# Kernel tuning notes

Hardware: AMD Instinct MI355X
Metric: run time of the kernel (lower is better)

Reference implementation:

```python
import jax, jax.numpy as jnp
import numpy as np

B, CIN, T, H, W = 2, 512, 8, 32, 32
COUT = 512

def conv2d(x, w, b):
    # x: (B, C, H, W), w: (O, I, kh, kw) -> (B, O, H, W), SAME padding
    y = jax.lax.conv_general_dilated(x, w, (1, 1), 'SAME',
        dimension_numbers=('NCHW', 'OIHW', 'NCHW'))
    return y + b[None, :, None, None]

def convlstm(x, w, b, wci, wcf, wco):
    # x: (B, C, T, H, W) -> (B, Cout, T, H, W); peepholes wci/wcf/wco: (Cout, H, W)
    bb, c, t, hh, ww = x.shape
    cout = wci.shape[0]
    h0 = jnp.zeros((bb, cout, hh, ww), x.dtype)

    def step(carry, xt):
        Hp, Cp = carry
        z = conv2d(jnp.concatenate([xt, Hp], axis=1), w, b)  # (B, 4*Cout, H, W)
        ic, fc, cc, oc = jnp.split(z, 4, axis=1)
        i = jax.nn.sigmoid(ic + wci * Cp)
        f = jax.nn.sigmoid(fc + wcf * Cp)
        Cn = f * Cp + i * jax.nn.relu(cc)   # activation='relu'
        o = jax.nn.sigmoid(oc + wco * Cn)
        Hn = o * jax.nn.relu(Cn)
        return (Hn, Cn), Hn

    (_, _), hs = jax.lax.scan(step, (h0, h0), jnp.moveaxis(x, 2, 0))
    return jnp.moveaxis(hs, 0, 2)  # (B, Cout, T, H, W)

def setup_inputs():
    key = jax.random.key(0)
    ks = jax.random.split(key, 16)
    inp = {'x': jax.random.normal(ks[0], (B, CIN, T, H, W), jnp.float32)}
    for l in range(3):
        k = ks[1 + 5 * l: 6 + 5 * l]
        inp['conv_w%d' % (l + 1)] = jax.random.normal(k[0], (4 * COUT, CIN + COUT, 3, 3), jnp.float32) * 0.02
        inp['conv_b%d' % (l + 1)] = jnp.zeros((4 * COUT,), jnp.float32)
        inp['wci%d' % (l + 1)] = jax.random.normal(k[1], (COUT, H, W), jnp.float32) * 0.02
        inp['wcf%d' % (l + 1)] = jax.random.normal(k[2], (COUT, H, W), jnp.float32) * 0.02
        inp['wco%d' % (l + 1)] = jax.random.normal(k[3], (COUT, H, W), jnp.float32) * 0.02
    return inp

def reference(x, conv_w1, conv_b1, wci1, wcf1, wco1,
              conv_w2, conv_b2, wci2, wcf2, wco2,
              conv_w3, conv_b3, wci3, wcf3, wco3):
    y = convlstm(x, conv_w1, conv_b1, wci1, wcf1, wco1)
    y = convlstm(y, conv_w2, conv_b2, wci2, wcf2, wco2)
    y = convlstm(y, conv_w3, conv_b3, wci3, wcf3, wco3)
    # Sigmoid on last time step: output[:, :, -1] -> (B, Cout, H, W)
    return jax.nn.sigmoid(y[:, :, -1])
```

## Files before the change

### kernel.cpp

```cpp
#include <hip/hip_runtime.h>

typedef unsigned short u16;
typedef __bf16 bf16x8 __attribute__((ext_vector_type(8)));
typedef float f32x4 __attribute__((ext_vector_type(4)));

#define T_STEPS 8
#define PLANE 1156
#define ROWB 2176

__device__ __forceinline__ u16 f2bf(float f) {
    unsigned u = __float_as_uint(f);
    return (u16)((u + 0x7fff + ((u >> 16) & 1)) >> 16);
}
__device__ __forceinline__ float sigmoidf(float x) {
    return 1.f / (1.f + expf(-x));
}
__device__ __forceinline__ void gl_lds16(const void* g, void* l) {
    __builtin_amdgcn_global_load_lds(
        (const __attribute__((address_space(1))) void*)g,
        (__attribute__((address_space(3))) void*)l, 16, 0, 0);
}

__global__ void repack_w(const float* __restrict__ w,
                         u16* __restrict__ wx, u16* __restrict__ wh) {
    int g = blockIdx.x * 256 + threadIdx.x;
    int co_in = g & 127; g >>= 7;
    int quad  = g & 3;   g >>= 2;
    int kt    = g % 144; g /= 144;
    int co_blk = g & 15; g >>= 4;
    int part = g;
    int co = co_blk * 128 + co_in;
    int cc = kt / 9, r = kt - cc * 9;
    int ci = cc * 32 + quad * 8;
    const float* src = w + ((size_t)co * 1024 + (size_t)part * 512 + ci) * 9 + r;
    u16* dst = (part ? wh : wx) +
               ((((size_t)co_blk * 144 + kt) * 4 + quad) * 128 + co_in) * 8;
    union { u16 u[8]; uint4 v; } tmp;
#pragma unroll
    for (int j = 0; j < 8; j++) tmp.u[j] = f2bf(src[(size_t)j * 9]);
    *(uint4*)dst = tmp.v;
}

__global__ __launch_bounds__(256) void pretransform_x(
    const float* __restrict__ x, u16* __restrict__ Xp) {
    const int bt = blockIdx.x >> 5;
    const int y  = blockIdx.x & 31;
    const int b  = bt >> 3;
    const int xx = threadIdx.x & 31, cg0 = threadIdx.x >> 5;
    const float* src = x + ((size_t)(b * 512) * T_STEPS + (bt & 7)) * 1024
                         + y * 32 + xx;
    u16* dst = Xp + (((size_t)bt * 34 + y + 1) * 34 + (xx + 1)) * 512;
#pragma unroll
    for (int it = 0; it < 8; ++it) {
        const int cig = cg0 + it * 8;
        union { u16 u[8]; uint4 v; } pk;
#pragma unroll
        for (int j = 0; j < 8; ++j)
            pk.u[j] = f2bf(src[(size_t)(cig * 8 + j) * 8192]);
        *(uint4*)(dst + cig * 8) = pk.v;
    }
}

template<bool XMODE>
__global__ __launch_bounds__(512, 4) void conv_gemm(
    const u16* __restrict__ Wp, const u16* __restrict__ Xp, int t0,
    float* __restrict__ Z, int ldz) {
    __shared__ __align__(16) u16 Bt[2][6528];

    const int tid = threadIdx.x;
    const int GX  = XMODE ? 32 : 16;
    const int nwg = GX * 16;
    const int bid = blockIdx.y * GX + blockIdx.x;
    const int swz = (bid & 7) * (nwg >> 3) + (bid >> 3);
    const int co_blk = swz / GX;
    const int nblk   = swz - co_blk * GX;
    const int n0 = nblk * 128;

    const int wave = tid >> 6, lane = tid & 63;
    const int wm = wave >> 1, wn = wave & 1;
    const int q_l = lane >> 4, m_l = lane & 15;

    const int plane = n0 >> 10;
    const int bb_ = XMODE ? (plane & 1) : plane;
    const int tt  = XMODE ? (t0 + (plane >> 1)) : t0;
    const int pyb = (n0 & 1023) >> 5;
    const u16* pbase = Xp + (size_t)(bb_ * T_STEPS + tt) * PLANE * 512;

    const int c0 = tid;
    const int p0 = c0 >> 2, sl0 = c0 & 3;
    const int yl0 = p0 / 34, xl0 = p0 - yl0 * 34;
    const int src0 = ((pyb + yl0) * 34 + xl0) * 512 + ((sl0 ^ ((xl0 >> 1) & 3)) << 3);
    const int c1 = 512 + tid;
    const int p1 = c1 >> 2, sl1 = c1 & 3;
    const int yl1 = p1 / 34, xl1 = p1 - yl1 * 34;
    const int src1 = ((pyb + yl1) * 34 + xl1) * 512 + ((sl1 ^ ((xl1 >> 1) & 3)) << 3);
    const bool do1 = tid < 304;

    const bf16x8* Aq = (const bf16x8*)(const void*)
        ((const uint4*)(Wp + (size_t)co_blk * 144 * 4096)
         + (q_l * 128 + wm * 32 + m_l));

    int colb[2][3];
#pragma unroll
    for (int xh = 0; xh < 2; xh++)
#pragma unroll
        for (int rx = 0; rx < 3; rx++) {
            int xl = xh * 16 + m_l + rx;
            colb[xh][rx] = xl * 64 + ((q_l ^ ((xl >> 1) & 3)) << 4);
        }
    const int wnrow = wn * 2 * ROWB;

    f32x4 acc[2][4];
#pragma unroll
    for (int i = 0; i < 2; i++)
#pragma unroll
        for (int j = 0; j < 4; j++) acc[i][j] = (f32x4){0.f, 0.f, 0.f, 0.f};

    gl_lds16(pbase + src0, &Bt[0][c0 * 8]);
    if (do1) gl_lds16(pbase + src1, &Bt[0][c1 * 8]);
    bf16x8 areg[3][2];
    areg[0][0] = Aq[0];          areg[0][1] = Aq[16];
    areg[1][0] = Aq[512];        areg[1][1] = Aq[512 + 16];

    for (int cc = 0; cc < 16; ++cc) {
        const int cb = cc & 1;
        const char* btc = (const char*)&Bt[cb][0];
#pragma unroll
        for (int r = 0; r < 9; ++r) {
            const int kt = cc * 9 + r;
            if (r == 0) {
                asm volatile("" ::: "memory");
                asm volatile("s_waitcnt vmcnt(4)" ::: "memory");
                __builtin_amdgcn_s_barrier();
                asm volatile("" ::: "memory");
            }
            if (cc < 15 || r < 7) {
                areg[(r + 2) % 3][0] = Aq[(size_t)(kt + 2) * 512];
                areg[(r + 2) % 3][1] = Aq[(size_t)(kt + 2) * 512 + 16];
            }
            if (r == 1 && cc < 15) {
                const u16* gs = pbase + (cc + 1) * 32;
                gl_lds16(gs + src0, &Bt[cb ^ 1][c0 * 8]);
                if (do1) gl_lds16(gs + src1, &Bt[cb ^ 1][c1 * 8]);
            }
            const int ry = r / 3, rx = r % 3;
            bf16x8 af0 = areg[r % 3][0];
            bf16x8 af1 = areg[r % 3][1];
            bf16x8 bf0 = *(const bf16x8*)(btc + wnrow + (0 + ry) * ROWB + colb[0][rx]);
            bf16x8 bf1 = *(const bf16x8*)(btc + wnrow + (0 + ry) * ROWB + colb[1][rx]);
            bf16x8 bf2 = *(const bf16x8*)(btc + wnrow + (1 + ry) * ROWB + colb[0][rx]);
            bf16x8 bf3 = *(const bf16x8*)(btc + wnrow + (1 + ry) * ROWB + colb[1][rx]);
            __builtin_amdgcn_s_setprio(1);
            acc[0][0] = __builtin_amdgcn_mfma_f32_16x16x32_bf16(af0, bf0, acc[0][0], 0, 0, 0);
            acc[0][1] = __builtin_amdgcn_mfma_f32_16x16x32_bf16(af0, bf1, acc[0][1], 0, 0, 0);
            acc[0][2] = __builtin_amdgcn_mfma_f32_16x16x32_bf16(af0, bf2, acc[0][2], 0, 0, 0);
            acc[0][3] = __builtin_amdgcn_mfma_f32_16x16x32_bf16(af0, bf3, acc[0][3], 0, 0, 0);
            acc[1][0] = __builtin_amdgcn_mfma_f32_16x16x32_bf16(af1, bf0, acc[1][0], 0, 0, 0);
            acc[1][1] = __builtin_amdgcn_mfma_f32_16x16x32_bf16(af1, bf1, acc[1][1], 0, 0, 0);
            acc[1][2] = __builtin_amdgcn_mfma_f32_16x16x32_bf16(af1, bf2, acc[1][2], 0, 0, 0);
            acc[1][3] = __builtin_amdgcn_mfma_f32_16x16x32_bf16(af1, bf3, acc[1][3], 0, 0, 0);
            __builtin_amdgcn_s_setprio(0);
        }
    }

#pragma unroll
    for (int mt = 0; mt < 2; mt++)
#pragma unroll
        for (int nt = 0; nt < 4; nt++)
#pragma unroll
            for (int reg = 0; reg < 4; reg++) {
                int co = co_blk * 128 + wm * 32 + mt * 16 + q_l * 4 + reg;
                int n  = n0 + wn * 64 + nt * 16 + m_l;
                float* zp = &Z[(size_t)co * ldz + n];
                if (XMODE) *zp = acc[mt][nt][reg];
                else       *zp += acc[mt][nt][reg];
            }
}

__global__ __launch_bounds__(256) void gates_kernel(
    const float* __restrict__ zx, int nxoff,
    const float* __restrict__ bias,
    const float* __restrict__ wci, const float* __restrict__ wcf,
    const float* __restrict__ wco,
    float* __restrict__ C, int is_first,
    u16* __restrict__ Yp, int t,
    float* __restrict__ outp) {
    __shared__ u16 Hs[16][136];
    const int tid = threadIdx.x;
    const int s0  = blockIdx.x * 128;
    const int co0 = blockIdx.y * 16;
    const int b   = blockIdx.z;
    const int sl = tid & 127, ch = tid >> 7;
    const int s = s0 + sl;

#pragma unroll
    for (int k = 0; k < 8; ++k) {
        const int co = co0 + k * 2 + ch;
        const size_t zi_ = (size_t)co * 4096 + nxoff + b * 1024 + s;
        float zi = zx[zi_]                       + bias[co];
        float zf = zx[zi_ + (size_t)512 * 4096]  + bias[co + 512];
        float zc = zx[zi_ + (size_t)1024 * 4096] + bias[co + 1024];
        float zo = zx[zi_ + (size_t)1536 * 4096] + bias[co + 1536];
        const size_t ci_ = ((size_t)b * 512 + co) * 1024 + s;
        float Cp = is_first ? 0.f : C[ci_];
        const int ps = co * 1024 + s;
        float gi = sigmoidf(zi + wci[ps] * Cp);
        float gf = sigmoidf(zf + wcf[ps] * Cp);
        float Cn = gf * Cp + gi * fmaxf(zc, 0.f);
        float go = sigmoidf(zo + wco[ps] * Cn);
        float Hn = go * fmaxf(Cn, 0.f);
        C[ci_] = Cn;
        Hs[k * 2 + ch][sl] = f2bf(Hn);
        if (outp) outp[ci_] = sigmoidf(Hn);
    }
    __syncthreads();
    const int sl2 = tid & 127, half = tid >> 7;
    const int s2 = s0 + sl2;
    const int yp = (s2 >> 5) + 1, xp = (s2 & 31) + 1;
    u16* dst = Yp + (((size_t)(b * T_STEPS + t) * 34 + yp) * 34 + xp) * 512
                  + co0 + half * 8;
    union { u16 u[8]; uint4 v; } pk;
#pragma unroll
    for (int j = 0; j < 8; ++j) pk.u[j] = Hs[half * 8 + j][sl2];
    *(uint4*)dst = pk.v;
}

extern "C" void kernel_launch(void* const* d_in, const int* in_sizes, int n_in,
                              void* d_out, int out_size, void* d_ws, size_t ws_size,
                              hipStream_t stream) {
    const float* x = (const float*)d_in[0];

    char* ws = (char*)d_ws;
    size_t off = 0;
    auto carve = [&](size_t bytes) { char* p = ws + off; off += (bytes + 255) & ~(size_t)255; return p; };

    u16*   Wx   = (u16*)  carve((size_t)16 * 144 * 4096 * 2);
    u16*   Wh   = (u16*)  carve((size_t)16 * 144 * 4096 * 2);
    float* Zx   = (float*)carve((size_t)2048 * 4096 * 4);
    float* Cbuf = (float*)carve((size_t)2 * 512 * 1024 * 4);
    const size_t PADB = (size_t)16 * PLANE * 512 * 2;
    u16*   Yp1  = (u16*)  carve(PADB);
    u16*   Yp2  = (u16*)  carve(PADB);
    (void)ws_size; (void)in_sizes; (void)n_in; (void)out_size;

    hipMemsetAsync(Yp1, 0, PADB, stream);
    hipMemsetAsync(Yp2, 0, PADB, stream);
    pretransform_x<<<512, 256, 0, stream>>>(x, Yp2);

    for (int l = 0; l < 3; ++l) {
        const float* w    = (const float*)d_in[1 + 5 * l];
        const float* bias = (const float*)d_in[2 + 5 * l];
        const float* wci  = (const float*)d_in[3 + 5 * l];
        const float* wcf  = (const float*)d_in[4 + 5 * l];
        const float* wco  = (const float*)d_in[5 + 5 * l];
        const u16* inl = (l == 0) ? Yp2 : (l == 1 ? Yp1 : Yp2);
        u16* Ycur      = (l == 0) ? Yp1 : (l == 1 ? Yp2 : Yp1);

        repack_w<<<9216, 256, 0, stream>>>(w, Wx, Wh);

        for (int t = 0; t < T_STEPS; ++t) {
            if ((t & 1) == 0)
                conv_gemm<true><<<dim3(32, 16), 512, 0, stream>>>(
                    Wx, inl, t, Zx, 4096);
            if (t > 0)
                conv_gemm<false><<<dim3(16, 16), 512, 0, stream>>>(
                    Wh, Ycur, t - 1, Zx + (size_t)(t & 1) * 2048, 4096);
            float* outp = (l == 2 && t == T_STEPS - 1) ? (float*)d_out : nullptr;
            gates_kernel<<<dim3(8, 32, 2), 256, 0, stream>>>(
                Zx, (t & 1) * 2048, bias, wci, wcf, wco,
                Cbuf, (t == 0) ? 1 : 0, Ycur, t, outp);
        }
    }
}
```

Measured before the change: 2.266 ms.

## Double output-channel tile for input conv and double-buffer LDS B-fragment reads

The input-projection GEMM now computes 256 output channels per workgroup (MF=4) instead of 128, halving the grid and the number of times each activation tile is staged into LDS. The weight repack lays out the input half with a 256-channel block stride to match. B fragments from LDS are now prefetched one tap ahead into a register double buffer, and the barrier/waitcnt is hoisted per channel chunk with counts adjusted for the extra A loads. Launch bounds drop to 2 waves-per-EU occupancy to allow the larger accumulator and register footprint, trading occupancy for reuse.

New measurement: 2.214 ms. 2.3% less time.

```diff
diff --git a/kernel.cpp b/kernel.cpp
--- a/kernel.cpp
+++ b/kernel.cpp
@@ -24,17 +24,26 @@
 __global__ void repack_w(const float* __restrict__ w,
                          u16* __restrict__ wx, u16* __restrict__ wh) {
     int g = blockIdx.x * 256 + threadIdx.x;
-    int co_in = g & 127; g >>= 7;
-    int quad  = g & 3;   g >>= 2;
-    int kt    = g % 144; g /= 144;
-    int co_blk = g & 15; g >>= 4;
-    int part = g;
-    int co = co_blk * 128 + co_in;
+    const int HALF = 1179648;
+    int part = g >= HALF;
+    int gg = part ? g - HALF : g;
+    int co_in, co_blk, quad, kt, co; u16* dst;
+    if (!part) {
+        co_in = gg & 255; gg >>= 8;
+        quad  = gg & 3;   gg >>= 2;
+        kt = gg % 144; co_blk = gg / 144;
+        co = co_blk * 256 + co_in;
+        dst = wx + ((((size_t)co_blk * 144 + kt) * 4 + quad) * 256 + co_in) * 8;
+    } else {
+        co_in = gg & 127; gg >>= 7;
+        quad  = gg & 3;   gg >>= 2;
+        kt = gg % 144; co_blk = gg / 144;
+        co = co_blk * 128 + co_in;
+        dst = wh + ((((size_t)co_blk * 144 + kt) * 4 + quad) * 128 + co_in) * 8;
+    }
     int cc = kt / 9, r = kt - cc * 9;
     int ci = cc * 32 + quad * 8;
     const float* src = w + ((size_t)co * 1024 + (size_t)part * 512 + ci) * 9 + r;
-    u16* dst = (part ? wh : wx) +
-               ((((size_t)co_blk * 144 + kt) * 4 + quad) * 128 + co_in) * 8;
     union { u16 u[8]; uint4 v; } tmp;
 #pragma unroll
     for (int j = 0; j < 8; j++) tmp.u[j] = f2bf(src[(size_t)j * 9]);
@@ -61,19 +70,28 @@
     }
 }
 
+#define READB(dstv, btcp, rr) {                                              \
+    const int ry_ = (rr) / 3, rx_ = (rr) % 3;                                \
+    dstv[0] = *(const bf16x8*)((btcp) + wnrow + (0 + ry_) * ROWB + colb[0][rx_]); \
+    dstv[1] = *(const bf16x8*)((btcp) + wnrow + (0 + ry_) * ROWB + colb[1][rx_]); \
+    dstv[2] = *(const bf16x8*)((btcp) + wnrow + (1 + ry_) * ROWB + colb[0][rx_]); \
+    dstv[3] = *(const bf16x8*)((btcp) + wnrow + (1 + ry_) * ROWB + colb[1][rx_]); }
+
 template<bool XMODE>
-__global__ __launch_bounds__(512, 4) void conv_gemm(
+__global__ __launch_bounds__(512, 2) void conv_gemm(
     const u16* __restrict__ Wp, const u16* __restrict__ Xp, int t0,
     float* __restrict__ Z, int ldz) {
+    constexpr int MF   = XMODE ? 4 : 2;
+    constexpr int COIN = XMODE ? 256 : 128;
+    constexpr int KSTR = 4 * COIN;
+
     __shared__ __align__(16) u16 Bt[2][6528];
 
     const int tid = threadIdx.x;
-    const int GX  = XMODE ? 32 : 16;
-    const int nwg = GX * 16;
-    const int bid = blockIdx.y * GX + blockIdx.x;
-    const int swz = (bid & 7) * (nwg >> 3) + (bid >> 3);
-    const int co_blk = swz / GX;
-    const int nblk   = swz - co_blk * GX;
+    const int bid = blockIdx.y * (XMODE ? 32 : 16) + blockIdx.x;
+    const int swz = (bid & 7) * 32 + (bid >> 3);
+    const int co_blk = XMODE ? (swz >> 5) : (swz >> 4);
+    const int nblk   = XMODE ? (swz & 31) : (swz & 15);
     const int n0 = nblk * 128;
 
     const int wave = tid >> 6, lane = tid & 63;
@@ -96,9 +114,8 @@
     const int src1 = ((pyb + yl1) * 34 + xl1) * 512 + ((sl1 ^ ((xl1 >> 1) & 3)) << 3);
     const bool do1 = tid < 304;
 
-    const bf16x8* Aq = (const bf16x8*)(const void*)
-        ((const uint4*)(Wp + (size_t)co_blk * 144 * 4096)
-         + (q_l * 128 + wm * 32 + m_l));
+    const uint4* Aq = (const uint4*)Wp + (size_t)co_blk * 144 * KSTR
+                      + q_l * COIN + wm * (MF * 16) + m_l;
 
     int colb[2][3];
 #pragma unroll
@@ -110,66 +127,74 @@
         }
     const int wnrow = wn * 2 * ROWB;
 
-    f32x4 acc[2][4];
-#pragma unroll
-    for (int i = 0; i < 2; i++)
+    f32x4 acc[MF][4];
+#pragma unroll
+    for (int i = 0; i < MF; i++)
 #pragma unroll
         for (int j = 0; j < 4; j++) acc[i][j] = (f32x4){0.f, 0.f, 0.f, 0.f};
+
+    bf16x8 areg[3][MF], breg[2][4];
 
     gl_lds16(pbase + src0, &Bt[0][c0 * 8]);
     if (do1) gl_lds16(pbase + src1, &Bt[0][c1 * 8]);
-    bf16x8 areg[3][2];
-    areg[0][0] = Aq[0];          areg[0][1] = Aq[16];
-    areg[1][0] = Aq[512];        areg[1][1] = Aq[512 + 16];
+#pragma unroll
+    for (int mt = 0; mt < MF; ++mt) {
+        areg[0][mt] = *(const bf16x8*)(Aq + mt * 16);
+        areg[1][mt] = *(const bf16x8*)(Aq + KSTR + mt * 16);
+    }
 
     for (int cc = 0; cc < 16; ++cc) {
         const int cb = cc & 1;
         const char* btc = (const char*)&Bt[cb][0];
+        asm volatile("" ::: "memory");
+        if (cc == 0) {
+            if (XMODE) asm volatile("s_waitcnt vmcnt(8)" ::: "memory");
+            else       asm volatile("s_waitcnt vmcnt(4)" ::: "memory");
+        } else {
+            if (XMODE) asm volatile("s_waitcnt vmcnt(28)" ::: "memory");
+            else       asm volatile("s_waitcnt vmcnt(14)" ::: "memory");
+        }
+        __builtin_amdgcn_s_barrier();
+        asm volatile("" ::: "memory");
+        READB(breg[0], btc, 0);
 #pragma unroll
         for (int r = 0; r < 9; ++r) {
             const int kt = cc * 9 + r;
-            if (r == 0) {
-                asm volatile("" ::: "memory");
-                asm volatile("s_waitcnt vmcnt(4)" ::: "memory");
-                __builtin_amdgcn_s_barrier();
-                asm volatile("" ::: "memory");
-            }
             if (cc < 15 || r < 7) {
-                areg[(r + 2) % 3][0] = Aq[(size_t)(kt + 2) * 512];
-                areg[(r + 2) % 3][1] = Aq[(size_t)(kt + 2) * 512 + 16];
+#pragma unroll
+                for (int mt = 0; mt < MF; ++mt)
+                    areg[(r + 2) % 3][mt] =
+                        *(const bf16x8*)(Aq + (size_t)(kt + 2) * KSTR + mt * 16);
             }
             if (r == 1 && cc < 15) {
                 const u16* gs = pbase + (cc + 1) * 32;
                 gl_lds16(gs + src0, &Bt[cb ^ 1][c0 * 8]);
                 if (do1) gl_lds16(gs + src1, &Bt[cb ^ 1][c1 * 8]);
             }
-            const int ry = r / 3, rx = r % 3;
-            bf16x8 af0 = areg[r % 3][0];
-            bf16x8 af1 = areg[r % 3][1];
-            bf16x8 bf0 = *(const bf16x8*)(btc + wnrow + (0 + ry) * ROWB + colb[0][rx]);
-            bf16x8 bf1 = *(const bf16x8*)(btc + wnrow + (0 + ry) * ROWB + colb[1][rx]);
-            bf16x8 bf2 = *(const bf16x8*)(btc + wnrow + (1 + ry) * ROWB + colb[0][rx]);
-            bf16x8 bf3 = *(const bf16x8*)(btc + wnrow + (1 + ry) * ROWB + colb[1][rx]);
+            if (r < 8) READB(breg[(r + 1) & 1], btc, (r + 1));
             __builtin_amdgcn_s_setprio(1);
-            acc[0][0] = __builtin_amdgcn_mfma_f32_16x16x32_bf16(af0, bf0, acc[0][0], 0, 0, 0);
-            acc[0][1] = __builtin_amdgcn_mfma_f32_16x16x32_bf16(af0, bf1, acc[0][1], 0, 0, 0);
-            acc[0][2] = __builtin_amdgcn_mfma_f32_16x16x32_bf16(af0, bf2, acc[0][2], 0, 0, 0);
-            acc[0][3] = __builtin_amdgcn_mfma_f32_16x16x32_bf16(af0, bf3, acc[0][3], 0, 0, 0);
-            acc[1][0] = __builtin_amdgcn_mfma_f32_16x16x32_bf16(af1, bf0, acc[1][0], 0, 0, 0);
-            acc[1][1] = __builtin_amdgcn_mfma_f32_16x16x32_bf16(af1, bf1, acc[1][1], 0, 0, 0);
-            acc[1][2] = __builtin_amdgcn_mfma_f32_16x16x32_bf16(af1, bf2, acc[1][2], 0, 0, 0);
-            acc[1][3] = __builtin_amdgcn_mfma_f32_16x16x32_bf16(af1, bf3, acc[1][3], 0, 0, 0);
+#pragma unroll
+            for (int mt = 0; mt < MF; ++mt) {
+                acc[mt][0] = __builtin_amdgcn_mfma_f32_16x16x32_bf16(
+                    areg[r % 3][mt], breg[r & 1][0], acc[mt][0], 0, 0, 0);
+                acc[mt][1] = __builtin_amdgcn_mfma_f32_16x16x32_bf16(
+                    areg[r % 3][mt], breg[r & 1][1], acc[mt][1], 0, 0, 0);
+                acc[mt][2] = __builtin_amdgcn_mfma_f32_16x16x32_bf16(
+                    areg[r % 3][mt], breg[r & 1][2], acc[mt][2], 0, 0, 0);
+                acc[mt][3] = __builtin_amdgcn_mfma_f32_16x16x32_bf16(
+                    areg[r % 3][mt], breg[r & 1][3], acc[mt][3], 0, 0, 0);
+            }
             __builtin_amdgcn_s_setprio(0);
         }
     }
 
 #pragma unroll
-    for (int mt = 0; mt < 2; mt++)
+    for (int mt = 0; mt < MF; mt++)
 #pragma unroll
         for (int nt = 0; nt < 4; nt++)
 #pragma unroll
             for (int reg = 0; reg < 4; reg++) {
-                int co = co_blk * 128 + wm * 32 + mt * 16 + q_l * 4 + reg;
+                int co = co_blk * COIN + wm * (MF * 16) + mt * 16 + q_l * 4 + reg;
                 int n  = n0 + wn * 64 + nt * 16 + m_l;
                 float* zp = &Z[(size_t)co * ldz + n];
                 if (XMODE) *zp = acc[mt][nt][reg];
@@ -234,7 +259,7 @@
     size_t off = 0;
     auto carve = [&](size_t bytes) { char* p = ws + off; off += (bytes + 255) & ~(size_t)255; return p; };
 
-    u16*   Wx   = (u16*)  carve((size_t)16 * 144 * 4096 * 2);
+    u16*   Wx   = (u16*)  carve((size_t)8 * 144 * 8192 * 2);
     u16*   Wh   = (u16*)  carve((size_t)16 * 144 * 4096 * 2);
     float* Zx   = (float*)carve((size_t)2048 * 4096 * 4);
     float* Cbuf = (float*)carve((size_t)2 * 512 * 1024 * 4);
@@ -260,7 +285,7 @@
 
         for (int t = 0; t < T_STEPS; ++t) {
             if ((t & 1) == 0)
-                conv_gemm<true><<<dim3(32, 16), 512, 0, stream>>>(
+                conv_gemm<true><<<dim3(32, 8), 512, 0, stream>>>(
                     Wx, inl, t, Zx, 4096);
             if (t > 0)
                 conv_gemm<false><<<dim3(16, 16), 512, 0, stream>>>(
```

## Fuse recurrent H-convolution with LSTM gate epilogue and prefetch LDS fragments

Applied to the files above, without the earlier changes.

The recurrent conv GEMM and the gates kernel become one kernel, hconv_gates, for t>0. Wh is repacked so each 128-row block holds the i/f/c/o gates for the same 32 channels, which lets the epilogue compute the cell update in registers. This removes the read-modify-write of Z and a separate gates launch. Both conv kernels also double-buffer B fragments from LDS one step ahead and relax the vmcnt wait. The cost is a different wave tiling (4x2 MFMA tiles per wave), more registers at occupancy 2, and extra global loads of zx and the peepholes in the epilogue.

After: 2.240 ms. Within noise of the previous version (-1.1%).

```diff
diff --git a/kernel.cpp b/kernel.cpp
--- a/kernel.cpp
+++ b/kernel.cpp
@@ -29,12 +29,18 @@
     int kt    = g % 144; g /= 144;
     int co_blk = g & 15; g >>= 4;
     int part = g;
-    int co = co_blk * 128 + co_in;
     int cc = kt / 9, r = kt - cc * 9;
     int ci = cc * 32 + quad * 8;
+    int co;
+    u16* dst;
+    if (!part) {
+        co = co_blk * 128 + co_in;
+        dst = wx + ((((size_t)co_blk * 144 + kt) * 4 + quad) * 128 + co_in) * 8;
+    } else {
+        co = ((co_in >> 4) & 3) * 512 + co_blk * 32 + (co_in >> 6) * 16 + (co_in & 15);
+        dst = wh + ((((size_t)co_blk * 144 + kt) * 4 + quad) * 128 + co_in) * 8;
+    }
     const float* src = w + ((size_t)co * 1024 + (size_t)part * 512 + ci) * 9 + r;
-    u16* dst = (part ? wh : wx) +
-               ((((size_t)co_blk * 144 + kt) * 4 + quad) * 128 + co_in) * 8;
     union { u16 u[8]; uint4 v; } tmp;
 #pragma unroll
     for (int j = 0; j < 8; j++) tmp.u[j] = f2bf(src[(size_t)j * 9]);
@@ -61,19 +67,28 @@
     }
 }
 
-template<bool XMODE>
+#define READB4(dstv, btcp, rr) {                                             \
+    const int ry_ = (rr) / 3, rx_ = (rr) % 3;                                \
+    dstv[0] = *(const bf16x8*)((btcp) + wnrow + (0 + ry_) * ROWB + colb[0][rx_]); \
+    dstv[1] = *(const bf16x8*)((btcp) + wnrow + (0 + ry_) * ROWB + colb[1][rx_]); \
+    dstv[2] = *(const bf16x8*)((btcp) + wnrow + (1 + ry_) * ROWB + colb[0][rx_]); \
+    dstv[3] = *(const bf16x8*)((btcp) + wnrow + (1 + ry_) * ROWB + colb[1][rx_]); }
+
+#define READB2(dstv, btcp, rr) {                                             \
+    const int ry_ = (rr) / 3, rx_ = (rr) % 3;                                \
+    dstv[0] = *(const bf16x8*)((btcp) + wnrow + ry_ * ROWB + colb[0][rx_]);  \
+    dstv[1] = *(const bf16x8*)((btcp) + wnrow + ry_ * ROWB + colb[1][rx_]); }
+
 __global__ __launch_bounds__(512, 4) void conv_gemm(
     const u16* __restrict__ Wp, const u16* __restrict__ Xp, int t0,
-    float* __restrict__ Z, int ldz) {
+    float* __restrict__ Z) {
     __shared__ __align__(16) u16 Bt[2][6528];
 
     const int tid = threadIdx.x;
-    const int GX  = XMODE ? 32 : 16;
-    const int nwg = GX * 16;
-    const int bid = blockIdx.y * GX + blockIdx.x;
-    const int swz = (bid & 7) * (nwg >> 3) + (bid >> 3);
-    const int co_blk = swz / GX;
-    const int nblk   = swz - co_blk * GX;
+    const int bid = blockIdx.y * 32 + blockIdx.x;
+    const int swz = (bid & 7) * 64 + (bid >> 3);
+    const int co_blk = swz >> 5;
+    const int nblk   = swz & 31;
     const int n0 = nblk * 128;
 
     const int wave = tid >> 6, lane = tid & 63;
@@ -81,8 +96,8 @@
     const int q_l = lane >> 4, m_l = lane & 15;
 
     const int plane = n0 >> 10;
-    const int bb_ = XMODE ? (plane & 1) : plane;
-    const int tt  = XMODE ? (t0 + (plane >> 1)) : t0;
+    const int bb_ = plane & 1;
+    const int tt  = t0 + (plane >> 1);
     const int pyb = (n0 & 1023) >> 5;
     const u16* pbase = Xp + (size_t)(bb_ * T_STEPS + tt) * PLANE * 512;
 
@@ -96,9 +111,8 @@
     const int src1 = ((pyb + yl1) * 34 + xl1) * 512 + ((sl1 ^ ((xl1 >> 1) & 3)) << 3);
     const bool do1 = tid < 304;
 
-    const bf16x8* Aq = (const bf16x8*)(const void*)
-        ((const uint4*)(Wp + (size_t)co_blk * 144 * 4096)
-         + (q_l * 128 + wm * 32 + m_l));
+    const uint4* Aq = (const uint4*)Wp + (size_t)co_blk * 144 * 512
+                      + q_l * 128 + wm * 32 + m_l;
 
     int colb[2][3];
 #pragma unroll
@@ -116,49 +130,47 @@
 #pragma unroll
         for (int j = 0; j < 4; j++) acc[i][j] = (f32x4){0.f, 0.f, 0.f, 0.f};
 
+    bf16x8 areg[3][2], breg[2][4];
+
     gl_lds16(pbase + src0, &Bt[0][c0 * 8]);
     if (do1) gl_lds16(pbase + src1, &Bt[0][c1 * 8]);
-    bf16x8 areg[3][2];
-    areg[0][0] = Aq[0];          areg[0][1] = Aq[16];
-    areg[1][0] = Aq[512];        areg[1][1] = Aq[512 + 16];
+#pragma unroll
+    for (int mt = 0; mt < 2; ++mt) {
+        areg[0][mt] = *(const bf16x8*)(Aq + mt * 16);
+        areg[1][mt] = *(const bf16x8*)(Aq + 512 + mt * 16);
+    }
 
     for (int cc = 0; cc < 16; ++cc) {
         const int cb = cc & 1;
         const char* btc = (const char*)&Bt[cb][0];
+        asm volatile("" ::: "memory");
+        if (cc == 0) asm volatile("s_waitcnt vmcnt(4)" ::: "memory");
+        else         asm volatile("s_waitcnt vmcnt(14)" ::: "memory");
+        __builtin_amdgcn_s_barrier();
+        asm volatile("" ::: "memory");
+        READB4(breg[0], btc, 0);
 #pragma unroll
         for (int r = 0; r < 9; ++r) {
             const int kt = cc * 9 + r;
-            if (r == 0) {
-                asm volatile("" ::: "memory");
-                asm volatile("s_waitcnt vmcnt(4)" ::: "memory");
-                __builtin_amdgcn_s_barrier();
-                asm volatile("" ::: "memory");
-            }
             if (cc < 15 || r < 7) {
-                areg[(r + 2) % 3][0] = Aq[(size_t)(kt + 2) * 512];
-                areg[(r + 2) % 3][1] = Aq[(size_t)(kt + 2) * 512 + 16];
+#pragma unroll
+                for (int mt = 0; mt < 2; ++mt)
+                    areg[(r + 2) % 3][mt] =
+                        *(const bf16x8*)(Aq + (size_t)(kt + 2) * 512 + mt * 16);
             }
             if (r == 1 && cc < 15) {
                 const u16* gs = pbase + (cc + 1) * 32;
                 gl_lds16(gs + src0, &Bt[cb ^ 1][c0 * 8]);
                 if (do1) gl_lds16(gs + src1, &Bt[cb ^ 1][c1 * 8]);
             }
-            const int ry = r / 3, rx = r % 3;
-            bf16x8 af0 = areg[r % 3][0];
-            bf16x8 af1 = areg[r % 3][1];
-            bf16x8 bf0 = *(const bf16x8*)(btc + wnrow + (0 + ry) * ROWB + colb[0][rx]);
-            bf16x8 bf1 = *(const bf16x8*)(btc + wnrow + (0 + ry) * ROWB + colb[1][rx]);
-            bf16x8 bf2 = *(const bf16x8*)(btc + wnrow + (1 + ry) * ROWB + colb[0][rx]);
-            bf16x8 bf3 = *(const bf16x8*)(btc + wnrow + (1 + ry) * ROWB + colb[1][rx]);
+            if (r < 8) READB4(breg[(r + 1) & 1], btc, (r + 1));
             __builtin_amdgcn_s_setprio(1);
-            acc[0][0] = __builtin_amdgcn_mfma_f32_16x16x32_bf16(af0, bf0, acc[0][0], 0, 0, 0);
-            acc[0][1] = __builtin_amdgcn_mfma_f32_16x16x32_bf16(af0, bf1, acc[0][1], 0, 0, 0);
-            acc[0][2] = __builtin_amdgcn_mfma_f32_16x16x32_bf16(af0, bf2, acc[0][2], 0, 0, 0);
-            acc[0][3] = __builtin_amdgcn_mfma_f32_16x16x32_bf16(af0, bf3, acc[0][3], 0, 0, 0);
-            acc[1][0] = __builtin_amdgcn_mfma_f32_16x16x32_bf16(af1, bf0, acc[1][0], 0, 0, 0);
-            acc[1][1] = __builtin_amdgcn_mfma_f32_16x16x32_bf16(af1, bf1, acc[1][1], 0, 0, 0);
-            acc[1][2] = __builtin_amdgcn_mfma_f32_16x16x32_bf16(af1, bf2, acc[1][2], 0, 0, 0);
-            acc[1][3] = __builtin_amdgcn_mfma_f32_16x16x32_bf16(af1, bf3, acc[1][3], 0, 0, 0);
+#pragma unroll
+            for (int mt = 0; mt < 2; ++mt)
+#pragma unroll
+                for (int nt = 0; nt < 4; ++nt)
+                    acc[mt][nt] = __builtin_amdgcn_mfma_f32_16x16x32_bf16(
+                        areg[r % 3][mt], breg[r & 1][nt], acc[mt][nt], 0, 0, 0);
             __builtin_amdgcn_s_setprio(0);
         }
     }
@@ -171,10 +183,140 @@
             for (int reg = 0; reg < 4; reg++) {
                 int co = co_blk * 128 + wm * 32 + mt * 16 + q_l * 4 + reg;
                 int n  = n0 + wn * 64 + nt * 16 + m_l;
-                float* zp = &Z[(size_t)co * ldz + n];
-                if (XMODE) *zp = acc[mt][nt][reg];
-                else       *zp += acc[mt][nt][reg];
-            }
+                Z[(size_t)co * 4096 + n] = acc[mt][nt][reg];
+            }
+}
+
+__global__ __launch_bounds__(512, 2) void hconv_gates(
+    const u16* __restrict__ Wp, const u16* __restrict__ Yprev, int tprev,
+    const float* __restrict__ zx, int nxoff,
+    const float* __restrict__ bias,
+    const float* __restrict__ wci, const float* __restrict__ wcf,
+    const float* __restrict__ wco,
+    float* __restrict__ C, u16* __restrict__ Yp, int t,
+    float* __restrict__ outp) {
+    __shared__ __align__(16) u16 Bt[2][6528];
+
+    const int tid = threadIdx.x;
+    const int bid = blockIdx.y * 16 + blockIdx.x;
+    const int swz = (bid & 7) * 32 + (bid >> 3);
+    const int co_blk = swz >> 4;
+    const int nblk   = swz & 15;
+    const int n0 = nblk * 128;
+
+    const int wave = tid >> 6, lane = tid & 63;
+    const int wm = wave >> 2, wn = wave & 3;
+    const int q_l = lane >> 4, m_l = lane & 15;
+
+    const int b = n0 >> 10;
+    const int pyb = (n0 & 1023) >> 5;
+    const u16* pbase = Yprev + (size_t)(b * T_STEPS + tprev) * PLANE * 512;
+
+    const int c0 = tid;
+    const int p0 = c0 >> 2, sl0 = c0 & 3;
+    const int yl0 = p0 / 34, xl0 = p0 - yl0 * 34;
+    const int src0 = ((pyb + yl0) * 34 + xl0) * 512 + ((sl0 ^ ((xl0 >> 1) & 3)) << 3);
+    const int c1 = 512 + tid;
+    const int p1 = c1 >> 2, sl1 = c1 & 3;
+    const int yl1 = p1 / 34, xl1 = p1 - yl1 * 34;
+    const int src1 = ((pyb + yl1) * 34 + xl1) * 512 + ((sl1 ^ ((xl1 >> 1) & 3)) << 3);
+    const bool do1 = tid < 304;
+
+    const uint4* Aq = (const uint4*)Wp + (size_t)co_blk * 144 * 512
+                      + q_l * 128 + wm * 64 + m_l;
+
+    int colb[2][3];
+#pragma unroll
+    for (int nt = 0; nt < 2; nt++)
+#pragma unroll
+        for (int rx = 0; rx < 3; rx++) {
+            int xl = nt * 16 + m_l + rx;
+            colb[nt][rx] = xl * 64 + ((q_l ^ ((xl >> 1) & 3)) << 4);
+        }
+    const int wnrow = wn * ROWB;
+
+    f32x4 acc[4][2];
+#pragma unroll
+    for (int i = 0; i < 4; i++)
+#pragma unroll
+        for (int j = 0; j < 2; j++) acc[i][j] = (f32x4){0.f, 0.f, 0.f, 0.f};
+
+    bf16x8 areg[3][4], breg[2][2];
+
+    gl_lds16(pbase + src0, &Bt[0][c0 * 8]);
+    if (do1) gl_lds16(pbase + src1, &Bt[0][c1 * 8]);
+#pragma unroll
+    for (int mt = 0; mt < 4; ++mt) {
+        areg[0][mt] = *(const bf16x8*)(Aq + mt * 16);
+        areg[1][mt] = *(const bf16x8*)(Aq + 512 + mt * 16);
+    }
+
+    for (int cc = 0; cc < 16; ++cc) {
+        const int cb = cc & 1;
+        const char* btc = (const char*)&Bt[cb][0];
+        asm volatile("" ::: "memory");
+        if (cc == 0) asm volatile("s_waitcnt vmcnt(8)" ::: "memory");
+        else         asm volatile("s_waitcnt vmcnt(28)" ::: "memory");
+        __builtin_amdgcn_s_barrier();
+        asm volatile("" ::: "memory");
+        READB2(breg[0], btc, 0);
+#pragma unroll
+        for (int r = 0; r < 9; ++r) {
+            const int kt = cc * 9 + r;
+            if (cc < 15 || r < 7) {
+#pragma unroll
+                for (int mt = 0; mt < 4; ++mt)
+                    areg[(r + 2) % 3][mt] =
+                        *(const bf16x8*)(Aq + (size_t)(kt + 2) * 512 + mt * 16);
+            }
+            if (r == 1 && cc < 15) {
+                const u16* gs = pbase + (cc + 1) * 32;
+                gl_lds16(gs + src0, &Bt[cb ^ 1][c0 * 8]);
+                if (do1) gl_lds16(gs + src1, &Bt[cb ^ 1][c1 * 8]);
+            }
+            if (r < 8) READB2(breg[(r + 1) & 1], btc, (r + 1));
+            __builtin_amdgcn_s_setprio(1);
+#pragma unroll
+            for (int g = 0; g < 4; ++g) {
+                acc[g][0] = __builtin_amdgcn_mfma_f32_16x16x32_bf16(
+                    areg[r % 3][g], breg[r & 1][0], acc[g][0], 0, 0, 0);
+                acc[g][1] = __builtin_amdgcn_mfma_f32_16x16x32_bf16(
+                    areg[r % 3][g], breg[r & 1][1], acc[g][1], 0, 0, 0);
+            }
+            __builtin_amdgcn_s_setprio(0);
+        }
+    }
+
+    const int chb = co_blk * 32 + wm * 16 + q_l * 4;
+#pragma unroll
+    for (int nt = 0; nt < 2; ++nt) {
+        const int n = n0 + wn * 32 + nt * 16 + m_l;
+        const int s = n & 1023;
+        const int zcol = nxoff + n;
+        const int yp = (s >> 5) + 1, xp = (s & 31) + 1;
+        union { u16 u[4]; uint2 v; } yv;
+#pragma unroll
+        for (int reg = 0; reg < 4; ++reg) {
+            const int ch = chb + reg;
+            float zi = acc[0][nt][reg] + zx[(size_t)ch * 4096 + zcol]          + bias[ch];
+            float zf = acc[1][nt][reg] + zx[(size_t)(512 + ch) * 4096 + zcol]  + bias[512 + ch];
+            float zc = acc[2][nt][reg] + zx[(size_t)(1024 + ch) * 4096 + zcol] + bias[1024 + ch];
+            float zo = acc[3][nt][reg] + zx[(size_t)(1536 + ch) * 4096 + zcol] + bias[1536 + ch];
+            const size_t ci_ = (size_t)(b * 512 + ch) * 1024 + s;
+            const int ps = ch * 1024 + s;
+            float Cp = C[ci_];
+            float gi = sigmoidf(zi + wci[ps] * Cp);
+            float gf = sigmoidf(zf + wcf[ps] * Cp);
+            float Cn = gf * Cp + gi * fmaxf(zc, 0.f);
+            float go = sigmoidf(zo + wco[ps] * Cn);
+            float Hn = go * fmaxf(Cn, 0.f);
+            C[ci_] = Cn;
+            yv.u[reg] = f2bf(Hn);
+            if (outp) outp[ci_] = sigmoidf(Hn);
+        }
+        u16* yd = Yp + (((size_t)(b * T_STEPS + t) * 34 + yp) * 34 + xp) * 512 + chb;
+        *(uint2*)yd = yv.v;
+    }
 }
 
 __global__ __launch_bounds__(256) void gates_kernel(
@@ -260,15 +402,16 @@
 
         for (int t = 0; t < T_STEPS; ++t) {
             if ((t & 1) == 0)
-                conv_gemm<true><<<dim3(32, 16), 512, 0, stream>>>(
-                    Wx, inl, t, Zx, 4096);
-            if (t > 0)
-                conv_gemm<false><<<dim3(16, 16), 512, 0, stream>>>(
-                    Wh, Ycur, t - 1, Zx + (size_t)(t & 1) * 2048, 4096);
+                conv_gemm<<<dim3(32, 16), 512, 0, stream>>>(Wx, inl, t, Zx);
             float* outp = (l == 2 && t == T_STEPS - 1) ? (float*)d_out : nullptr;
-            gates_kernel<<<dim3(8, 32, 2), 256, 0, stream>>>(
-                Zx, (t & 1) * 2048, bias, wci, wcf, wco,
-                Cbuf, (t == 0) ? 1 : 0, Ycur, t, outp);
-        }
-    }
-}
+            if (t == 0) {
+                gates_kernel<<<dim3(8, 32, 2), 256, 0, stream>>>(
+                    Zx, 0, bias, wci, wcf, wco, Cbuf, 1, Ycur, 0, outp);
+            } else {
+                hconv_gates<<<dim3(16, 16), 512, 0, stream>>>(
+                    Wh, Ycur, t - 1, Zx, (t & 1) * 2048,
+                    bias, wci, wcf, wco, Cbuf, Ycur, t, outp);
+            }
+        }
+    }
+}
```
